# Kernel optimization log

Hardware: AMD Instinct MI355X
Metric: run time of the kernel (lower is better)

The kernel has to match this reference:

```python
import jax, jax.numpy as jnp
import numpy as np

IN_F = 4096
OUT_F = 4096
N_TOK = 8192  # batch 4 * seq 2048 tokens


def setup_inputs() -> dict:
    key = jax.random.key(0)
    k1, k2, k3 = jax.random.split(key, 3)
    x = jax.random.normal(k1, (N_TOK, IN_F), dtype=jnp.float16)
    # int4-range quantized weights stored as int8, as produced by quantize_weight()
    weight_q = jax.random.randint(k2, (OUT_F, IN_F), -8, 8, dtype=jnp.int8)
    # positive per-output-channel scales (weight_max/7, clamped >= 1e-5)
    weight_scale = (jax.random.uniform(k3, (OUT_F,), dtype=jnp.float32) * 0.01 + 1e-4).astype(jnp.float16)
    return {"x": x, "weight_q": weight_q, "weight_scale": weight_scale}


def reference(x, weight_q, weight_scale):
    # per-token symmetric int4 activation quantization
    x_max = jnp.max(jnp.abs(x), axis=-1, keepdims=True)          # [N, 1]
    x_scale = jnp.maximum(x_max / jnp.float16(7.0), jnp.float16(1e-5))
    x_q = jnp.clip(jnp.round(x / x_scale), -8, 7)                # int4 values in fp16
    # fp32 GEMM emulating int4xint4 matmul
    acc = jnp.matmul(x_q.astype(jnp.float32), weight_q.astype(jnp.float32).T)  # [N, OUT]
    # dequant: (x_scale * weight_scale) is [N, OUT]; unsqueeze(0) as in original
    scale = (x_scale.astype(jnp.float32) * weight_scale.astype(jnp.float32)[None, :])[None]  # [1, N, OUT]
    out = acc * scale                                            # [1, N, OUT]
    return out.astype(x.dtype)
```

## Files before the change

kernel.cpp:

```cpp
#include <hip/hip_runtime.h>
#include <hip/hip_fp16.h>
#include <stdint.h>

#define K_DIM 4096
#define N_OUT 4096
#define BM 256
#define BN 256
#define BKB 64

typedef __attribute__((ext_vector_type(4))) int int32x4;
typedef __attribute__((ext_vector_type(16))) int int32x16;

__global__ __launch_bounds__(256) void quant_x(const float* __restrict__ x,
                                               int8_t* __restrict__ xq,
                                               float* __restrict__ xs) {
  const int row = blockIdx.x;
  const int t = threadIdx.x;
  const float4* xr = (const float4*)(x + (size_t)row * K_DIM);
  float4 v[4];
  float m = 0.f;
#pragma unroll
  for (int i = 0; i < 4; ++i) {
    v[i] = xr[t * 4 + i];
    m = fmaxf(m, fmaxf(fmaxf(fabsf(v[i].x), fabsf(v[i].y)),
                       fmaxf(fabsf(v[i].z), fabsf(v[i].w))));
  }
#pragma unroll
  for (int off = 32; off > 0; off >>= 1) m = fmaxf(m, __shfl_xor(m, off));
  __shared__ float wmax[4];
  if ((t & 63) == 0) wmax[t >> 6] = m;
  __syncthreads();
  m = fmaxf(fmaxf(wmax[0], wmax[1]), fmaxf(wmax[2], wmax[3]));

  const float eps = 1.0013580322265625e-05f;
  const float xscale = fmaxf(m / 7.0f, eps);
  if (t == 0) xs[row] = xscale;

  uint32_t p[4];
#pragma unroll
  for (int g = 0; g < 4; ++g) {
    const float* fv = (const float*)&v[g];
    uint32_t w = 0;
#pragma unroll
    for (int j = 0; j < 4; ++j) {
      float r = rintf(fv[j] / xscale);
      r = fminf(fmaxf(r, -8.f), 7.f);
      w |= ((uint32_t)(uint8_t)(int8_t)(int)r) << (8 * j);
    }
    p[g] = w;
  }
  *(uint4*)(xq + (size_t)row * K_DIM + t * 16) = *(uint4*)p;
}

__global__ __launch_bounds__(256) void pack_w(const int* __restrict__ w,
                                              uint32_t* __restrict__ wqf) {
  const int c = blockIdx.x * 256 + threadIdx.x;
  const int blk = c >> 6;
  const int l = c & 63;
  const int row = ((blk >> 7) << 5) + (l & 31);
  const int k = ((blk & 127) << 5) + ((l >> 5) << 4);
  const int4* src = (const int4*)(w + (size_t)row * K_DIM + k);
  uint32_t p[4];
#pragma unroll
  for (int g = 0; g < 4; ++g) {
    const int4 v = src[g];
    p[g] = (uint32_t)(v.x & 255) | ((uint32_t)(v.y & 255) << 8) |
           ((uint32_t)(v.z & 255) << 16) | ((uint32_t)(v.w & 255) << 24);
  }
  *(uint4*)(wqf + (size_t)c * 4) = *(uint4*)p;
}

__global__ __launch_bounds__(512, 2) void gemm_w4a4(
    const int8_t* __restrict__ xq, const uint8_t* __restrict__ wqf,
    const float* __restrict__ xs, const float* __restrict__ wscale,
    float* __restrict__ out, int M) {
  __shared__ uint8_t lds[2][16384];

  const int bid = blockIdx.x;
  const int xcd = bid & 7;
  const int i_loc = bid >> 3;
  const int mt = xcd * 4 + (i_loc & 3);
  const int nt = i_loc >> 2;
  const int tm = mt * BM;
  const int tn = nt * BN;

  const int t = threadIdx.x;
  const int l = t & 63;
  const int wv = t >> 6;
  const int wm = wv >> 2;
  const int wn = wv & 3;

  const uint8_t* gA = (const uint8_t*)xq +
                      (size_t)(tm + wv * 32 + (l & 31)) * K_DIM +
                      ((l >> 5) << 4);
  const int nfrag0 = nt * 8 + wn * 2;
  const uint8_t* gB0 = wqf + ((size_t)(nfrag0 * 128) << 10) + l * 16;
  const uint8_t* gB1 = wqf + ((size_t)((nfrag0 + 1) * 128) << 10) + l * 16;

  int32x16 acc[4][2] = {};

  auto stageA2 = [&](int buf, int ss) {
#pragma unroll
    for (int j = 0; j < 2; ++j) {
      __builtin_amdgcn_global_load_lds(
          (const __attribute__((address_space(1))) uint32_t*)(
              gA + ss * BKB + j * 32),
          (__attribute__((address_space(3))) uint32_t*)(
              &lds[buf][(wv * 2 + j) * 1024 + l * 16]),
          16, 0, 0);
    }
  };

  auto loadB = [&](int32x4 (&b)[4], int ss) {
    b[0] = *(const int32x4*)(gB0 + ((size_t)(ss * 2 + 0) << 10));
    b[1] = *(const int32x4*)(gB0 + ((size_t)(ss * 2 + 1) << 10));
    b[2] = *(const int32x4*)(gB1 + ((size_t)(ss * 2 + 0) << 10));
    b[3] = *(const int32x4*)(gB1 + ((size_t)(ss * 2 + 1) << 10));
  };

#define PHASE_OPEN()                                    \
  __builtin_amdgcn_s_barrier();                         \
  asm volatile("s_waitcnt lgkmcnt(0)" ::: "memory");    \
  __builtin_amdgcn_sched_barrier(0);                    \
  __builtin_amdgcn_s_setprio(1);

#define PHASE_CLOSE()                                   \
  __builtin_amdgcn_s_setprio(0);

  const int nsteps = K_DIM / BKB;

  auto do_step = [&](int s, int32x4 (&bCur)[4], int32x4 (&bNext)[4]) {
    const int buf = s & 1;
    const uint8_t* aB = &lds[buf][wm * 8192 + l * 16];

    int32x4 a[4];
#pragma unroll
    for (int m = 0; m < 4; ++m)
      a[m] = *(const int32x4*)(aB + m * 2048 + 0 * 1024);
    stageA2(buf ^ 1, (s + 1) & 63);
    PHASE_OPEN()
#pragma unroll
    for (int m = 0; m < 4; ++m) {
      acc[m][0] = __builtin_amdgcn_mfma_i32_32x32x32_i8(a[m], bCur[0],
                                                        acc[m][0], 0, 0, 0);
      acc[m][1] = __builtin_amdgcn_mfma_i32_32x32x32_i8(a[m], bCur[2],
                                                        acc[m][1], 0, 0, 0);
    }
    PHASE_CLOSE()
    __builtin_amdgcn_s_barrier();

    int32x4 c[4];
#pragma unroll
    for (int m = 0; m < 4; ++m)
      c[m] = *(const int32x4*)(aB + m * 2048 + 1 * 1024);
    loadB(bNext, (s + 1) & 63);
    PHASE_OPEN()
#pragma unroll
    for (int m = 0; m < 4; ++m) {
      acc[m][0] = __builtin_amdgcn_mfma_i32_32x32x32_i8(c[m], bCur[1],
                                                        acc[m][0], 0, 0, 0);
      acc[m][1] = __builtin_amdgcn_mfma_i32_32x32x32_i8(c[m], bCur[3],
                                                        acc[m][1], 0, 0, 0);
    }
    PHASE_CLOSE()
    asm volatile("s_waitcnt vmcnt(4)" ::: "memory");
    __builtin_amdgcn_s_barrier();
  };

  int32x4 bX[4], bY[4];
  stageA2(0, 0);
  asm volatile("" ::: "memory");
  loadB(bX, 0);
  asm volatile("s_waitcnt vmcnt(4)" ::: "memory");
  __builtin_amdgcn_s_barrier();

  for (int s = 0; s < nsteps; s += 2) {
    do_step(s, bX, bY);
    do_step(s + 1, bY, bX);
  }
  asm volatile("s_waitcnt vmcnt(0)" ::: "memory");

#undef PHASE_OPEN
#undef PHASE_CLOSE

  const int colbase = tn + wn * 64;
  const int rowbase = tm + wm * 128 + 4 * (l >> 5);
#pragma unroll
  for (int m = 0; m < 4; ++m) {
#pragma unroll
    for (int n = 0; n < 2; ++n) {
      const int col = colbase + n * 32 + (l & 31);
      const float wsc = wscale[col];
#pragma unroll
      for (int j = 0; j < 16; ++j) {
        const int row = rowbase + m * 32 + (j & 3) + 8 * (j >> 2);
        const float val = (float)acc[m][n][j] * (xs[row] * wsc);
        out[(size_t)row * N_OUT + col] = __half2float(__float2half(val));
      }
    }
  }
}

extern "C" void kernel_launch(void* const* d_in, const int* in_sizes, int n_in,
                              void* d_out, int out_size, void* d_ws, size_t ws_size,
                              hipStream_t stream) {
  const float* x = (const float*)d_in[0];
  const int* w = (const int*)d_in[1];
  const float* wsc = (const float*)d_in[2];
  float* out = (float*)d_out;

  const int M = in_sizes[0] / K_DIM;

  uint8_t* ws = (uint8_t*)d_ws;
  int8_t* xq = (int8_t*)ws;
  uint8_t* wqf = ws + (size_t)M * K_DIM;
  float* xs = (float*)(ws + (size_t)M * K_DIM + (size_t)N_OUT * K_DIM);

  quant_x<<<M, 256, 0, stream>>>(x, xq, xs);
  pack_w<<<(N_OUT * K_DIM / 16) / 256, 256, 0, stream>>>(w, (uint32_t*)wqf);
  gemm_w4a4<<<(M / BM) * (N_OUT / BN), 512, 0, stream>>>(
      xq, wqf, xs, wsc, out, M);
}
```

Baseline: 230.5 us.

## Stage B through LDS with triple-buffered pipeline and 256x128 tiles

Shrinks the GEMM tile from 256x256 to 256x128 and the block from 512 to 256 threads (4 waves in a 2x2 grid). Weight fragments are now loaded into LDS with global_load_lds instead of directly into registers, alongside A. A three-stage LDS ring buffer prefetches two K-steps ahead. The aim is to hide global latency better and raise block count, at the cost of extra LDS traffic, more total A re-reads across N tiles, and 72KB of LDS per block that may limit occupancy.

New measurement: 217.8 us. -5.5%, faster.

```diff
diff --git a/kernel.cpp b/kernel.cpp
--- a/kernel.cpp
+++ b/kernel.cpp
@@ -5,7 +5,7 @@
 #define K_DIM 4096
 #define N_OUT 4096
 #define BM 256
-#define BN 256
+#define BN 128
 #define BKB 64
 
 typedef __attribute__((ext_vector_type(4))) int int32x4;
@@ -70,11 +70,11 @@
   *(uint4*)(wqf + (size_t)c * 4) = *(uint4*)p;
 }
 
-__global__ __launch_bounds__(512, 2) void gemm_w4a4(
+__global__ __launch_bounds__(256, 2) void gemm_w4a4(
     const int8_t* __restrict__ xq, const uint8_t* __restrict__ wqf,
     const float* __restrict__ xs, const float* __restrict__ wscale,
     float* __restrict__ out, int M) {
-  __shared__ uint8_t lds[2][16384];
+  __shared__ uint8_t lds[3][24576];
 
   const int bid = blockIdx.x;
   const int xcd = bid & 7;
@@ -87,35 +87,40 @@
   const int t = threadIdx.x;
   const int l = t & 63;
   const int wv = t >> 6;
-  const int wm = wv >> 2;
-  const int wn = wv & 3;
-
-  const uint8_t* gA = (const uint8_t*)xq +
-                      (size_t)(tm + wv * 32 + (l & 31)) * K_DIM +
+  const int wm = wv >> 1;
+  const int wn = wv & 1;
+
+  const uint8_t* gA = (const uint8_t*)xq + (size_t)(tm + (l & 31)) * K_DIM +
                       ((l >> 5) << 4);
-  const int nfrag0 = nt * 8 + wn * 2;
-  const uint8_t* gB0 = wqf + ((size_t)(nfrag0 * 128) << 10) + l * 16;
-  const uint8_t* gB1 = wqf + ((size_t)((nfrag0 + 1) * 128) << 10) + l * 16;
+  const uint8_t* gB = wqf + (size_t)(nt * 4) * 131072 + (size_t)l * 16;
 
   int32x16 acc[4][2] = {};
 
-  auto stageA2 = [&](int buf, int ss) {
-#pragma unroll
-    for (int j = 0; j < 2; ++j) {
+  auto stageA4 = [&](int buf, int ss) {
+#pragma unroll
+    for (int q = 0; q < 4; ++q) {
+      const int bIdx = q * 4 + wv;
       __builtin_amdgcn_global_load_lds(
           (const __attribute__((address_space(1))) uint32_t*)(
-              gA + ss * BKB + j * 32),
+              gA + (size_t)((bIdx >> 1) * 32) * K_DIM + (bIdx & 1) * 32 +
+              ss * BKB),
           (__attribute__((address_space(3))) uint32_t*)(
-              &lds[buf][(wv * 2 + j) * 1024 + l * 16]),
+              &lds[buf][q * 4096 + t * 16]),
           16, 0, 0);
     }
   };
-
-  auto loadB = [&](int32x4 (&b)[4], int ss) {
-    b[0] = *(const int32x4*)(gB0 + ((size_t)(ss * 2 + 0) << 10));
-    b[1] = *(const int32x4*)(gB0 + ((size_t)(ss * 2 + 1) << 10));
-    b[2] = *(const int32x4*)(gB1 + ((size_t)(ss * 2 + 0) << 10));
-    b[3] = *(const int32x4*)(gB1 + ((size_t)(ss * 2 + 1) << 10));
+  auto stageB2 = [&](int buf, int ss) {
+#pragma unroll
+    for (int q = 0; q < 2; ++q) {
+      const int bIdx = q * 4 + wv;
+      __builtin_amdgcn_global_load_lds(
+          (const __attribute__((address_space(1))) uint32_t*)(
+              gB + (size_t)(bIdx >> 1) * 131072 +
+              ((size_t)(ss * 2 + (bIdx & 1)) << 10)),
+          (__attribute__((address_space(3))) uint32_t*)(
+              &lds[buf][16384 + q * 4096 + t * 16]),
+          16, 0, 0);
+    }
   };
 
 #define PHASE_OPEN()                                    \
@@ -129,54 +134,58 @@
 
   const int nsteps = K_DIM / BKB;
 
-  auto do_step = [&](int s, int32x4 (&bCur)[4], int32x4 (&bNext)[4]) {
-    const int buf = s & 1;
+  stageA4(0, 0);
+  stageB2(0, 0);
+  stageA4(1, 1);
+  stageB2(1, 1);
+  asm volatile("s_waitcnt vmcnt(6)" ::: "memory");
+  __builtin_amdgcn_s_barrier();
+
+  for (int s = 0; s < nsteps; ++s) {
+    const int buf = s % 3;
+    const int sbuf = (s + 2) % 3;
+    const int ss = (s + 2) & 63;
     const uint8_t* aB = &lds[buf][wm * 8192 + l * 16];
-
-    int32x4 a[4];
+    const uint8_t* bB = &lds[buf][16384 + wn * 4096 + l * 16];
+
+    int32x4 a[4], b0[2];
 #pragma unroll
     for (int m = 0; m < 4; ++m)
       a[m] = *(const int32x4*)(aB + m * 2048 + 0 * 1024);
-    stageA2(buf ^ 1, (s + 1) & 63);
+#pragma unroll
+    for (int n = 0; n < 2; ++n)
+      b0[n] = *(const int32x4*)(bB + n * 2048 + 0 * 1024);
+    stageA4(sbuf, ss);
     PHASE_OPEN()
 #pragma unroll
     for (int m = 0; m < 4; ++m) {
-      acc[m][0] = __builtin_amdgcn_mfma_i32_32x32x32_i8(a[m], bCur[0],
+      acc[m][0] = __builtin_amdgcn_mfma_i32_32x32x32_i8(a[m], b0[0],
                                                         acc[m][0], 0, 0, 0);
-      acc[m][1] = __builtin_amdgcn_mfma_i32_32x32x32_i8(a[m], bCur[2],
+      acc[m][1] = __builtin_amdgcn_mfma_i32_32x32x32_i8(a[m], b0[1],
                                                         acc[m][1], 0, 0, 0);
     }
     PHASE_CLOSE()
     __builtin_amdgcn_s_barrier();
 
-    int32x4 c[4];
+    int32x4 c[4], b1[2];
 #pragma unroll
     for (int m = 0; m < 4; ++m)
       c[m] = *(const int32x4*)(aB + m * 2048 + 1 * 1024);
-    loadB(bNext, (s + 1) & 63);
+#pragma unroll
+    for (int n = 0; n < 2; ++n)
+      b1[n] = *(const int32x4*)(bB + n * 2048 + 1 * 1024);
+    stageB2(sbuf, ss);
     PHASE_OPEN()
 #pragma unroll
     for (int m = 0; m < 4; ++m) {
-      acc[m][0] = __builtin_amdgcn_mfma_i32_32x32x32_i8(c[m], bCur[1],
+      acc[m][0] = __builtin_amdgcn_mfma_i32_32x32x32_i8(c[m], b1[0],
                                                         acc[m][0], 0, 0, 0);
-      acc[m][1] = __builtin_amdgcn_mfma_i32_32x32x32_i8(c[m], bCur[3],
+      acc[m][1] = __builtin_amdgcn_mfma_i32_32x32x32_i8(c[m], b1[1],
                                                         acc[m][1], 0, 0, 0);
     }
     PHASE_CLOSE()
-    asm volatile("s_waitcnt vmcnt(4)" ::: "memory");
+    asm volatile("s_waitcnt vmcnt(6)" ::: "memory");
     __builtin_amdgcn_s_barrier();
-  };
-
-  int32x4 bX[4], bY[4];
-  stageA2(0, 0);
-  asm volatile("" ::: "memory");
-  loadB(bX, 0);
-  asm volatile("s_waitcnt vmcnt(4)" ::: "memory");
-  __builtin_amdgcn_s_barrier();
-
-  for (int s = 0; s < nsteps; s += 2) {
-    do_step(s, bX, bY);
-    do_step(s + 1, bY, bX);
   }
   asm volatile("s_waitcnt vmcnt(0)" ::: "memory");
 
@@ -218,6 +227,6 @@
 
   quant_x<<<M, 256, 0, stream>>>(x, xq, xs);
   pack_w<<<(N_OUT * K_DIM / 16) / 256, 256, 0, stream>>>(w, (uint32_t*)wqf);
-  gemm_w4a4<<<(M / BM) * (N_OUT / BN), 512, 0, stream>>>(
+  gemm_w4a4<<<(M / BM) * (N_OUT / BN), 256, 0, stream>>>(
       xq, wqf, xs, wsc, out, M);
 }
```
